# Kernel optimization log

Measured on AMD Instinct MI355X. Metric: run time of the kernel, lower is better.

The kernel has to match this reference:

```python
import jax, jax.numpy as jnp
import numpy as np

# ---- straight-through binary quantizers (custom VJP matches torch autograd.Functions) ----
@jax.custom_vjp
def bq(x):
    return jnp.sign(x)
def _bq_fwd(x):
    return jnp.sign(x), x
def _bq_bwd(x, g):
    return (g * ((x > -1.0) & (x < 1.0)).astype(g.dtype),)
bq.defvjp(_bq_fwd, _bq_bwd)

@jax.custom_vjp
def bq_quad(x):
    return jnp.sign(x)
def _bqq_fwd(x):
    return jnp.sign(x), x
def _bqq_bwd(x, g):
    return (jnp.maximum(2.0 - jnp.abs(2.0 * x), 0.0) * g,)
bq_quad.defvjp(_bqq_fwd, _bqq_bwd)

def bilinear(x, W, s, b):
    # BiLinear: row-centered sign weights scaled by learned per-row factor, sign activations
    Wc = W - jnp.mean(W, axis=-1, keepdims=True)
    Wb = s * bq(Wc)                      # (out, in)
    return bq(x) @ Wb.T + b

def selective_scan(u, delta, A, Bs, Cs, D, delta_bias):
    # u, delta: (B,K,Dn,L); A: (K,Dn,N); Bs,Cs: (B,K,N,L); D, delta_bias: (K,Dn)
    Bn, K, Dn, L = u.shape
    N = A.shape[-1]
    delta = jax.nn.softplus(delta + delta_bias[None, :, :, None])
    def step(h, inp):
        ut, dt, Bt, Ct = inp             # (B,K,Dn),(B,K,Dn),(B,K,N),(B,K,N)
        dA = jnp.exp(dt[..., None] * A[None])
        h = dA * h + (dt * ut)[..., None] * Bt[:, :, None, :]
        y = jnp.einsum('bkdn,bkn->bkd', h, Ct)
        return h, y
    h0 = jnp.zeros((Bn, K, Dn, N), u.dtype)
    _, ys = jax.lax.scan(step, h0,
                         (u.transpose(3, 0, 1, 2), delta.transpose(3, 0, 1, 2),
                          Bs.transpose(3, 0, 1, 2), Cs.transpose(3, 0, 1, 2)))
    y = ys.transpose(1, 2, 3, 0)         # (B,K,Dn,L)
    return y + D[None, :, :, None] * u

def _forward(x, W_in, b_in, s_in, move0_b, conv_W, conv_b, rp_b0, prelu_a, rp_b1,
             Wl, bl, sl, Wd, bd, sd, dt_bias, A_logs, Ds, ln_w, ln_b, W_out, b_out, s_out):
    Bn, H, Wi, dm = x.shape
    Dn = conv_W.shape[0]
    K = 4
    N = A_logs.shape[1]
    R = Wd.shape[2]
    L = H * Wi
    xz = bilinear(x, W_in, s_in, b_in)                  # (B,H,W,2*Dn)
    xp, z = jnp.split(xz, 2, axis=-1)
    xc = xp.transpose(0, 3, 1, 2)                       # (B,Dn,H,W)
    # BConv2d: move0 bias -> sign (quad STE) -> binary conv -> RPReLU -> residual
    t = bq_quad(xc + move0_b[None, :, None, None])
    sc = jax.lax.stop_gradient(jnp.mean(jnp.abs(conv_W), axis=(1, 2, 3), keepdims=True))
    cw = jnp.clip(conv_W, -1.0, 1.0)
    Wb = jax.lax.stop_gradient(sc * jnp.sign(conv_W) - cw) + cw
    t = jax.lax.conv_general_dilated(t, Wb, (1, 1), [(1, 1), (1, 1)],
                                     dimension_numbers=('NCHW', 'OIHW', 'NCHW'))
    t = t + conv_b[None, :, None, None]
    t = t + rp_b0[None, :, None, None]
    t = jnp.where(t >= 0, t, prelu_a[None, :, None, None] * t)
    t = t + rp_b1[None, :, None, None] + xc
    xconv = jax.nn.silu(t)
    # 4-direction scan inputs
    x_flat = xconv.reshape(Bn, Dn, L)
    x_tr = xconv.transpose(0, 1, 3, 2).reshape(Bn, Dn, L)
    x_hwwh = jnp.stack([x_flat, x_tr], axis=1)
    xs = jnp.concatenate([x_hwwh, jnp.flip(x_hwwh, axis=-1)], axis=1)   # (B,K,Dn,L)
    # NOTE: torch does .view(B,L,-1) on contiguous (B,Dn,L) slices = raw reshape (not transpose)
    xin = xs.reshape(Bn, K, L, Dn)
    x_dbl = jax.vmap(bilinear, in_axes=(1, 0, 0, 0), out_axes=1)(xin, Wl, sl, bl)  # (B,K,L,R+2N)
    x_dbl = x_dbl.transpose(0, 1, 3, 2)                                 # (B,K,R+2N,L)
    dts_r, Bs, Cs = jnp.split(x_dbl, [R, R + N], axis=2)
    dts_in = dts_r.reshape(Bn, K, L, R)  # raw reshape, matches torch .view
    dts = jax.vmap(bilinear, in_axes=(1, 0, 0, 0), out_axes=1)(dts_in, Wd, sd, bd)  # (B,K,L,Dn)
    dts = dts.transpose(0, 1, 3, 2)                                     # (B,K,Dn,L)
    A = -jnp.exp(A_logs).reshape(K, Dn, N)
    out_y = selective_scan(xs, dts, A, Bs, Cs, Ds.reshape(K, Dn), dt_bias.reshape(K, Dn))
    inv_y = jnp.flip(out_y[:, 2:4], axis=-1)
    wh_y = out_y[:, 1].reshape(Bn, Dn, Wi, H).transpose(0, 1, 3, 2).reshape(Bn, Dn, L)
    invwh_y = inv_y[:, 1].reshape(Bn, Dn, Wi, H).transpose(0, 1, 3, 2).reshape(Bn, Dn, L)
    y = out_y[:, 0] + inv_y[:, 0] + wh_y + invwh_y                      # (B,Dn,L)
    y = y.transpose(0, 2, 1).reshape(Bn, H, Wi, Dn)
    mu = jnp.mean(y, axis=-1, keepdims=True)
    var = jnp.var(y, axis=-1, keepdims=True)
    y = (y - mu) / jnp.sqrt(var + 1e-5) * ln_w + ln_b                   # LayerNorm eps=1e-5
    y = y * jax.nn.silu(z)
    return bilinear(y, W_out, s_out, b_out)

def setup_inputs():
    key = jax.random.key(0)
    ks = jax.random.split(key, 12)
    B, H, Wi, dm = 4, 64, 64, 96
    Dn, N, R, K = 192, 16, 6, 4
    u = lambda k, sh, a: jax.random.uniform(k, sh, jnp.float32, -a, a)
    x = jax.random.normal(ks[0], (B, H, Wi, dm), jnp.float32)
    W_in = u(ks[1], (2 * Dn, dm), 0.015)
    b_in = u(ks[2], (2 * Dn,), 0.01)
    s_in = jnp.mean(jnp.abs(W_in), axis=1, keepdims=True)
    move0_b = jnp.zeros((Dn,), jnp.float32)
    conv_W = 0.05 * jax.random.normal(ks[3], (Dn, Dn, 3, 3), jnp.float32)
    conv_b = u(ks[4], (Dn,), 0.01)
    rp_b0 = jnp.zeros((Dn,), jnp.float32)
    prelu_a = 0.25 * jnp.ones((Dn,), jnp.float32)
    rp_b1 = jnp.zeros((Dn,), jnp.float32)
    Wl = u(ks[5], (K, R + 2 * N, Dn), 0.015)
    bl = u(ks[6], (K, R + 2 * N), 0.01)
    sl = jnp.mean(jnp.abs(Wl), axis=2, keepdims=True)
    std = R ** -0.5
    Wd = u(ks[7], (K, Dn, R), std)
    bd = u(ks[8], (K, Dn), 0.01)
    sd = jnp.mean(jnp.abs(Wd), axis=2, keepdims=True)
    dt = jnp.exp(jax.random.uniform(ks[9], (K * Dn,), jnp.float32)
                 * (np.log(0.1) - np.log(0.001)) + np.log(0.001))
    dt = jnp.clip(dt, 1e-4, None)
    dt_bias = dt + jnp.log(-jnp.expm1(-dt))
    A_logs = jnp.tile(jnp.log(jnp.arange(1, N + 1, dtype=jnp.float32))[None, :], (K * Dn, 1))
    Ds = jnp.ones((K * Dn,), jnp.float32)
    ln_w = jnp.ones((Dn,), jnp.float32)
    ln_b = jnp.zeros((Dn,), jnp.float32)
    W_out = u(ks[10], (dm, Dn), 0.015)
    b_out = u(ks[11], (dm,), 0.01)
    s_out = jnp.mean(jnp.abs(W_out), axis=1, keepdims=True)
    return dict(x=x, W_in=W_in, b_in=b_in, s_in=s_in, move0_b=move0_b, conv_W=conv_W,
                conv_b=conv_b, rp_b0=rp_b0, prelu_a=prelu_a, rp_b1=rp_b1, Wl=Wl, bl=bl,
                sl=sl, Wd=Wd, bd=bd, sd=sd, dt_bias=dt_bias, A_logs=A_logs, Ds=Ds,
                ln_w=ln_w, ln_b=ln_b, W_out=W_out, b_out=b_out, s_out=s_out)

def reference(x, W_in, b_in, s_in, move0_b, conv_W, conv_b, rp_b0, prelu_a, rp_b1,
              Wl, bl, sl, Wd, bd, sd, dt_bias, A_logs, Ds, ln_w, ln_b, W_out, b_out, s_out):
    return _forward(x, W_in, b_in, s_in, move0_b, conv_W, conv_b, rp_b0, prelu_a, rp_b1,
                    Wl, bl, sl, Wd, bd, sd, dt_bias, A_logs, Ds, ln_w, ln_b, W_out, b_out, s_out)
```

## Files before the change

### kernel.cpp

```cpp
#include <hip/hip_runtime.h>
#include <math.h>
#include <stdint.h>

#define BB 4
#define HH 64
#define WW2 64
#define DM 96
#define DN 192
#define KK 4
#define NN 16
#define RR 6
#define LL 4096
#define RN 38

#define LOG2E 1.4426950408889634f
#define LN2   0.6931471805599453f

#define OFF_WDB      0
#define OFF_WCS      4608
#define OFF_WAUX     15360
#define OFF_WSC      16896
#define OFF_WBIB     17088
#define OFF_WOUTB    18240
#define OFF_WLBB     18816
#define OFF_XBP      19728
#define OFF_PXS      19728
#define OFF_PXIN     412944
#define OFF_XP       462096
#define OFF_XCONV    3607824
#define OFF_XCT      6753552
#define OFF_HEND     462096
#define OFF_YA       9899280
#define OFF_SSUM     22482192

#define PLANE 4356
#define NCH 128
#define CHUNK 32

__device__ __forceinline__ float softplusf(float v) {
  return fmaxf(v, 0.f) + LN2 * log2f(1.f + exp2f(-fabsf(v) * LOG2E));
}
__device__ __forceinline__ float siluf(float v) {
  return v / (1.f + expf(-v));
}
__device__ __forceinline__ float waveAllSum(float s) {
  #pragma unroll
  for (int off = 32; off; off >>= 1) s += __shfl_xor(s, off, 64);
  return s;
}

__global__ __launch_bounds__(64) void k_prep(
    const float* __restrict__ W_in, const float* __restrict__ s_in,
    const float* __restrict__ W_out, const float* __restrict__ s_out,
    const float* __restrict__ Wl, const float* __restrict__ sl,
    const float* __restrict__ Wd, const float* __restrict__ sd,
    const float* __restrict__ convW, float* __restrict__ ws) {
  __shared__ float srow[1728];
  int r = blockIdx.x, lane = threadIdx.x;
  if (r < 384) {
    const float* row = W_in + r * DM;
    float s = 0.f;
    for (int c = lane; c < DM; c += 64) s += row[c];
    s = waveAllSum(s);
    float mean = s / (float)DM;
    if (lane < 3) {
      uint32_t wv = 0;
      #pragma unroll
      for (int i = 0; i < 32; ++i) wv |= (row[lane * 32 + i] - mean > 0.f ? 1u : 0u) << i;
      ((uint32_t*)(ws + OFF_WBIB))[r * 3 + lane] = wv;
    }
  } else if (r < 480) {
    int m = r - 384;
    const float* row = W_out + m * DN;
    float s = 0.f;
    for (int c = lane; c < DN; c += 64) s += row[c];
    s = waveAllSum(s);
    float mean = s / (float)DN;
    if (lane < 6) {
      uint32_t wv = 0;
      #pragma unroll
      for (int i = 0; i < 32; ++i) wv |= (row[lane * 32 + i] - mean > 0.f ? 1u : 0u) << i;
      ((uint32_t*)(ws + OFF_WOUTB))[m * 6 + lane] = wv;
    }
  } else if (r < 632) {
    int idx = r - 480;
    const float* row = Wl + idx * DN;
    float s = 0.f;
    for (int c = lane; c < DN; c += 64) s += row[c];
    s = waveAllSum(s);
    float mean = s / (float)DN;
    if (lane < 6) {
      uint32_t wv = 0;
      #pragma unroll
      for (int i = 0; i < 32; ++i) wv |= (row[lane * 32 + i] - mean > 0.f ? 1u : 0u) << i;
      ((uint32_t*)(ws + OFF_WLBB))[idx * 6 + lane] = wv;
    }
  } else if (r < 1400) {
    int idx = r - 632;
    const float* row = Wd + idx * RR;
    float s = (lane < RR) ? row[lane] : 0.f;
    s = waveAllSum(s);
    float mean = s / (float)RR;
    unsigned long long mb = __ballot((lane < RR) && (row[lane] - mean > 0.f));
    if (lane == 0) {
      ((uint32_t*)(ws + OFF_WDB))[idx] = (uint32_t)mb & 0x3Fu;
      (ws + OFF_WDB)[768 + idx] = sd[idx];
    }
  } else if (r < 1592) {
    int o = r - 1400;
    const float* row = convW + o * 1728;
    float s = 0.f;
    for (int j = lane; j < 1728; j += 64) {
      float v = row[j];
      srow[j] = v;
      s += fabsf(v);
    }
    s = waveAllSum(s);
    __syncthreads();
    float sc = s / 1728.f;
    uint32_t* wb = (uint32_t*)(ws + OFF_WCS);
    int* aux = (int*)(ws + OFF_WAUX);
    float* scf = ws + OFF_WSC;
    uint32_t word = 0;
    if (lane < 54) {
      int cw = lane / 9, tap = lane % 9;
      #pragma unroll
      for (int i = 0; i < 32; ++i)
        word |= (srow[(cw * 32 + i) * 9 + tap] > 0.f ? 1u : 0u) << i;
      wb[o * 56 + lane] = word;
    } else if (lane < 56) {
      wb[o * 56 + lane] = 0u;
    }
    int pc = (lane < 54) ? 2 * (int)__popc(word) - 32 : 0;
    int tapid = lane % 9;
    int wst = 0;
    #pragma unroll
    for (int cw = 0; cw < 6; ++cw) wst += __shfl(pc, cw * 9 + tapid, 64);
    int w_t[9];
    #pragma unroll
    for (int t9 = 0; t9 < 9; ++t9) w_t[t9] = __shfl(wst, t9, 64);
    if (lane == 0) {
      aux[o * 8 + 0] = w_t[0] + w_t[3] + w_t[6];
      aux[o * 8 + 1] = w_t[2] + w_t[5] + w_t[8];
      aux[o * 8 + 2] = w_t[0] + w_t[1] + w_t[2];
      aux[o * 8 + 3] = w_t[6] + w_t[7] + w_t[8];
      aux[o * 8 + 4] = w_t[0];
      aux[o * 8 + 5] = w_t[2];
      aux[o * 8 + 6] = w_t[6];
      aux[o * 8 + 7] = w_t[8];
      scf[o] = sc;
    }
  } else {
    int p = r - 1592;
    uint32_t* plane = (uint32_t*)(ws + OFF_XBP) + (size_t)p * PLANE;
    for (int i = lane; i < 66; i += 64) {
      plane[i] = 0u;
      plane[65 * 66 + i] = 0u;
    }
    for (int i = lane; i < 64; i += 64) {
      plane[(i + 1) * 66] = 0u;
      plane[(i + 1) * 66 + 65] = 0u;
    }
  }
}

__global__ __launch_bounds__(384) void k_bilin_in(
    const float* __restrict__ x, const float* __restrict__ b_in,
    const float* __restrict__ s_in, const float* __restrict__ move0,
    const float* __restrict__ ws, float* __restrict__ xp,
    uint32_t* __restrict__ pxin, uint32_t* __restrict__ xb) {
  __shared__ uint32_t spx[16 * 3];
  __shared__ float sxz[192 * 17];
  __shared__ float smv[DN];
  int p0 = blockIdx.x * 16;
  if (threadIdx.x < 48) {
    int pix = threadIdx.x / 3, wd = threadIdx.x % 3;
    const float* base = x + (size_t)(p0 + pix) * DM + wd * 32;
    uint32_t wv = 0;
    #pragma unroll
    for (int i = 0; i < 32; ++i) wv |= (base[i] > 0.f ? 1u : 0u) << i;
    spx[pix * 3 + wd] = wv;
  }
  if (threadIdx.x < DN) smv[threadIdx.x] = move0[threadIdx.x];
  __syncthreads();
  int half = threadIdx.x / 192;
  int o = threadIdx.x - half * 192;
  uint32_t w0, w1, w2;
  {
    const uint32_t* wb = (const uint32_t*)(ws + OFF_WBIB) + o * 3;
    w0 = wb[0]; w1 = wb[1]; w2 = wb[2];
  }
  float bias = b_in[o], sc = s_in[o];
  #pragma unroll
  for (int pp = 0; pp < 8; ++pp) {
    int pix = half * 8 + pp;
    int P = (int)__popc(spx[pix * 3 + 0] ^ w0) + (int)__popc(spx[pix * 3 + 1] ^ w1) +
            (int)__popc(spx[pix * 3 + 2] ^ w2);
    sxz[o * 17 + pix] = bias + sc * (float)(DM - 2 * P);
  }
  __syncthreads();
  int b = p0 >> 12, l0 = p0 & 4095;
  for (int f = threadIdx.x; f < DN * 16; f += 384) {
    int od = f >> 4, pix = f & 15;
    xp[((size_t)(b * DN + od)) * LL + l0 + pix] = sxz[od * 17 + pix];
  }
  if (threadIdx.x < 48) {
    int pix = threadIdx.x / 3, wd = threadIdx.x % 3;
    pxin[(size_t)(p0 + pix) * 3 + wd] = spx[pix * 3 + wd];
  }
  if (threadIdx.x < 96) {
    int pix = threadIdx.x / 6, cw = threadIdx.x % 6;
    uint32_t wv = 0;
    #pragma unroll
    for (int i = 0; i < 32; ++i) {
      int dch = cw * 32 + i;
      wv |= ((sxz[dch * 17 + pix] + smv[dch] > 0.f) ? 1u : 0u) << i;
    }
    int l = l0 + pix, h = l >> 6, w = l & 63;
    uint32_t* plane = xb + (size_t)(b * 6 + cw) * PLANE;
    plane[(h + 1) * 66 + 1 + w] = wv;
  }
}

__global__ __launch_bounds__(256) void k_conv(
    const uint32_t* __restrict__ xb, const float* __restrict__ xc,
    const uint32_t* __restrict__ wbits, const int* __restrict__ aux,
    const float* __restrict__ scf, const float* __restrict__ conv_b,
    const float* __restrict__ rp_b0, const float* __restrict__ prelu_a,
    const float* __restrict__ rp_b1, float* __restrict__ xconv) {
  int ocg = blockIdx.x & 3;
  int og = (blockIdx.x >> 2) & 3;
  int stripe = (blockIdx.x >> 4) & 15;
  int b = blockIdx.x >> 8;
  int w = threadIdx.x & 63, r = threadIdx.x >> 6;
  int h = stripe * 4 + r;
  int obase = og * 48 + ocg * 12;

  __shared__ uint32_t swb[12 * 56];
  __shared__ int saux[12 * 8];
  __shared__ float sconst[12 * 4];
  for (int i = threadIdx.x; i < 12 * 56; i += 256) swb[i] = wbits[obase * 56 + i];
  for (int i = threadIdx.x; i < 12 * 8; i += 256) saux[i] = aux[obase * 8 + i];
  if (threadIdx.x < 12) {
    int o = obase + threadIdx.x;
    sconst[threadIdx.x * 4 + 0] = scf[o];
    sconst[threadIdx.x * 4 + 1] = conv_b[o] + rp_b0[o];
    sconst[threadIdx.x * 4 + 2] = prelu_a[o];
    sconst[threadIdx.x * 4 + 3] = rp_b1[o];
  }

  uint32_t xw[6][9];
  const uint32_t* xpb = xb + (size_t)b * 6 * PLANE;
  #pragma unroll
  for (int cw = 0; cw < 6; ++cw) {
    const uint32_t* plane = xpb + cw * PLANE + (h + 1) * 66 + (w + 1);
    #pragma unroll
    for (int dy = 0; dy < 3; ++dy) {
      #pragma unroll
      for (int dx = 0; dx < 3; ++dx)
        xw[cw][dy * 3 + dx] = plane[(dy - 1) * 66 + (dx - 1)];
    }
  }
  bool isL = (w == 0), isR = (w == 63);
  bool isT = (h == 0), isB = (h == 63);
  const float* xcp = xc + ((size_t)(b * DN + obase)) * LL + h * 64 + w;
  float* xop = xconv + ((size_t)(b * DN + obase)) * LL + h * 64 + w;
  __syncthreads();

  #pragma unroll 1
  for (int oc = 0; oc < 12; ++oc) {
    const uint32_t* wp = &swb[oc * 56];
    int P = 0;
    #pragma unroll
    for (int cw = 0; cw < 6; ++cw) {
      int pp = 0;
      #pragma unroll
      for (int t = 0; t < 9; ++t) pp += (int)__popc(wp[cw * 9 + t] ^ xw[cw][t]);
      P += pp;
    }
    int corr = isL ? saux[oc * 8 + 0] : (isR ? saux[oc * 8 + 1] : 0);
    if (isT) {
      corr += saux[oc * 8 + 2];
      if (isL) corr -= saux[oc * 8 + 4];
      if (isR) corr -= saux[oc * 8 + 5];
    }
    if (isB) {
      corr += saux[oc * 8 + 3];
      if (isL) corr -= saux[oc * 8 + 6];
      if (isR) corr -= saux[oc * 8 + 7];
    }
    float acc = sconst[oc * 4 + 0] * (float)(1728 - 2 * P + corr);
    float t = acc + sconst[oc * 4 + 1];
    t = (t >= 0.f) ? t : sconst[oc * 4 + 2] * t;
    t += sconst[oc * 4 + 3] + *xcp;
    *xop = siluf(t);
    xcp += LL; xop += LL;
  }
}

__global__ __launch_bounds__(256) void k_bits_xpose(const float* __restrict__ xconv,
                                                    uint32_t* __restrict__ pxs,
                                                    float* __restrict__ xct) {
  __shared__ float tile[64][65];
  if (blockIdx.x < 768) {
    int bd = blockIdx.x;
    int b = bd / DN, dch = bd - b * DN;
    const float* img = xconv + (size_t)bd * LL;
    for (int i = threadIdx.x; i < LL; i += 256)
      tile[i >> 6][i & 63] = img[i];
    __syncthreads();
    int lane = threadIdx.x & 63;
    #pragma unroll
    for (int k = 0; k < 4; ++k) {
      size_t wbase = ((size_t)((b * KK + k) * DN + dch)) * 128;
      for (int j = threadIdx.x; j < LL; j += 256) {
        float v;
        if (k == 0)      v = tile[j >> 6][j & 63];
        else if (k == 1) v = tile[j & 63][j >> 6];
        else if (k == 2) { int t2 = 4095 - j; v = tile[t2 >> 6][t2 & 63]; }
        else             { int t2 = 4095 - j; v = tile[t2 & 63][t2 >> 6]; }
        unsigned long long m = __ballot(v > 0.f);
        if (lane == 0)       pxs[wbase + (j >> 5)] = (uint32_t)m;
        else if (lane == 32) pxs[wbase + (j >> 5)] = (uint32_t)(m >> 32);
      }
    }
  } else {
    int idx = blockIdx.x - 768;
    int ts = idx & 63;
    int rest = idx >> 6;
    int dg = rest % 3;
    int b = rest / 3;
    int d0 = dg * 64, t0 = ts * 64;
    for (int i = threadIdx.x; i < 4096; i += 256) {
      int dd = i >> 6, tt = i & 63;
      tile[dd][tt] = xconv[((size_t)(b * DN + d0 + dd)) * LL + t0 + tt];
    }
    __syncthreads();
    for (int i = threadIdx.x; i < 4096; i += 256) {
      int tt = i >> 6, dd = i & 63;
      xct[((size_t)(b * LL + t0 + tt)) * DN + d0 + dd] = tile[dd][tt];
    }
  }
}

__device__ __forceinline__ void rpowers(float r, float* a) {
  float r2 = r * r, r3 = r2 * r, r4 = r2 * r2, r8 = r4 * r4;
  a[0] = r;       a[1] = r2;      a[2] = r3;      a[3] = r4;
  a[4] = r4 * r;  a[5] = r4 * r2; a[6] = r4 * r3; a[7] = r8;
  a[8] = r8 * r;  a[9] = r8 * r2; a[10] = r8 * r3; a[11] = r8 * r4;
  a[12] = r8 * a[4]; a[13] = r8 * a[5]; a[14] = r8 * a[6]; a[15] = r8 * r8;
}

__device__ __forceinline__ int rowstep(int k) {
  return (k == 0) ? DN : (k == 1) ? 64 * DN : (k == 2) ? -DN : -64 * DN;
}
__device__ __forceinline__ int rowbase(int k, int tb) {
  int r0 = (k >= 2) ? (4095 - tb) : tb;
  if (k & 1) r0 = ((r0 & 63) << 6) | (r0 >> 6);
  return r0 * DN;
}

__global__ __launch_bounds__(192) void k_scan_a(
    const float* __restrict__ xct, const uint32_t* __restrict__ pxs,
    const float* __restrict__ ws, const float* __restrict__ bl,
    const float* __restrict__ sl, const float* __restrict__ bd,
    const float* __restrict__ dt_bias, const float* __restrict__ A_logs,
    float* __restrict__ hend, float* __restrict__ Ssum) {
  int c = blockIdx.x & (NCH - 1);
  int bk = blockIdx.x >> 7;
  int k = bk & 3, b = bk >> 2;
  int d = threadIdx.x;
  int t0 = c << 5;
  __shared__ uint32_t sdtm[CHUNK];
  __shared__ uint32_t spxr[CHUNK * 6];
  __shared__ uint32_t swl[RN * 6];
  __shared__ float sblv[RN], sslv[RN];
  __shared__ float4 sB4[CHUNK * 4];
  __shared__ float sDV[7 * 192], sR[7 * 192];
  float* sBf = (float*)sB4;
  const uint32_t* ppx = pxs + (size_t)bk * 24576;
  spxr[d] = ppx[t0 * 6 + d];
  for (int i = d; i < RN * 6; i += 192) swl[i] = ((const uint32_t*)(ws + OFF_WLBB))[k * RN * 6 + i];
  if (d < RN) {
    sblv[d] = bl[k * RN + d];
    sslv[d] = sl[k * RN + d];
  }
  __syncthreads();
  if (d < CHUNK) {
    uint32_t m = 0;
    int fbase = (t0 + d) * 6;
    #pragma unroll
    for (int r = 0; r < 6; ++r) {
      int f = fbase + r;
      int o = f >> 12, l = f & 4095;
      const uint32_t* prow = ppx + l * 6;
      int P = 0;
      #pragma unroll
      for (int j = 0; j < 6; ++j) P += (int)__popc(prow[j] ^ swl[o * 6 + j]);
      float val = sblv[o] + sslv[o] * (float)(DN - 2 * P);
      m |= (val > 0.f ? 1u : 0u) << r;
    }
    sdtm[d] = m;
  }
  for (int i = d; i < CHUNK * 16; i += 192) {
    int t = i >> 4, n = i & 15;
    int o = RR + n;
    int P = 0;
    #pragma unroll
    for (int j = 0; j < 6; ++j) P += (int)__popc(spxr[t * 6 + j] ^ swl[o * 6 + j]);
    sBf[t * 16 + n] = sblv[o] + sslv[o] * (float)(DN - 2 * P);
  }
  uint32_t w6 = ((const uint32_t*)(ws + OFF_WDB))[k * DN + d];
  float sdvv = (ws + OFF_WDB)[768 + k * DN + d];
  float biasd = bd[k * DN + d] + dt_bias[k * DN + d];
  #pragma unroll
  for (int pc = 0; pc < 7; ++pc) {
    float dv = softplusf(biasd + sdvv * (float)(RR - 2 * pc));
    sDV[pc * 192 + d] = dv;
    sR[pc * 192 + d] = exp2f(-dv * LOG2E);
  }
  float Araw[16];
  bool fok = true;
  {
    const float* ap = A_logs + (k * DN + d) * NN;
    #pragma unroll
    for (int n = 0; n < NN; ++n) {
      Araw[n] = -expf(ap[n]);
      fok = fok && (fabsf(Araw[n] + (float)(n + 1)) < 1e-3f);
    }
  }
  bool fastpath = (__ballot(fok) == ~0ull);
  float An[16];
  if (!fastpath) {
    #pragma unroll
    for (int n = 0; n < NN; ++n) An[n] = Araw[n] * LOG2E;
  }
  float h[16];
  #pragma unroll
  for (int n = 0; n < NN; ++n) h[n] = 0.f;
  float S = 0.f;
  int ubase = b * (LL * DN) + d;
  int rstep = rowstep(k);
  __syncthreads();
  #pragma unroll 1
  for (int seg = 0; seg < 4; ++seg) {
    int rbase = rowbase(k, t0 + seg * 8);
    float uu[8];
    #pragma unroll
    for (int i = 0; i < 8; ++i) uu[i] = xct[ubase + rbase + i * rstep];
    #pragma unroll
    for (int i = 0; i < 8; ++i) {
      int t = seg * 8 + i;
      float uv = uu[i];
      int pc = (int)__popc(sdtm[t] ^ w6);
      float dv = sDV[pc * 192 + d];
      S += dv;
      float du = dv * uv;
      if (fastpath) {
        float rv = sR[pc * 192 + d];
        float a[16];
        rpowers(rv, a);
        #pragma unroll
        for (int g = 0; g < 4; ++g) {
          float4 bv = sB4[t * 4 + g];
          h[4 * g + 0] = a[4 * g + 0] * h[4 * g + 0] + du * bv.x;
          h[4 * g + 1] = a[4 * g + 1] * h[4 * g + 1] + du * bv.y;
          h[4 * g + 2] = a[4 * g + 2] * h[4 * g + 2] + du * bv.z;
          h[4 * g + 3] = a[4 * g + 3] * h[4 * g + 3] + du * bv.w;
        }
      } else {
        #pragma unroll
        for (int g = 0; g < 4; ++g) {
          float4 bv = sB4[t * 4 + g];
          float a0 = exp2f(dv * An[4 * g + 0]);
          float a1 = exp2f(dv * An[4 * g + 1]);
          float a2 = exp2f(dv * An[4 * g + 2]);
          float a3 = exp2f(dv * An[4 * g + 3]);
          h[4 * g + 0] = a0 * h[4 * g + 0] + du * bv.x;
          h[4 * g + 1] = a1 * h[4 * g + 1] + du * bv.y;
          h[4 * g + 2] = a2 * h[4 * g + 2] + du * bv.z;
          h[4 * g + 3] = a3 * h[4 * g + 3] + du * bv.w;
        }
      }
    }
  }
  float* hp = hend + (size_t)c * 49152 + (size_t)(bk * DN + d) * 16;
  #pragma unroll
  for (int n = 0; n < NN; n += 4)
    *(float4*)(hp + n) = make_float4(h[n], h[n + 1], h[n + 2], h[n + 3]);
  Ssum[c * 3072 + bk * DN + d] = S;
}

__global__ __launch_bounds__(256) void k_scan_b(
    const float* __restrict__ A_logs, const float* __restrict__ Ssum,
    float* __restrict__ hend) {
  int tid = blockIdx.x * 256 + threadIdx.x;
  int bkd = tid >> 4, n = tid & 15;
  int bk = bkd / DN, d = bkd - bk * DN;
  int k = bk & 3;
  float An2 = -expf(A_logs[(k * DN + d) * NN + n]) * LOG2E;
  float h = 0.f;
  float Sc = Ssum[bkd];
  float he = hend[tid];
  #pragma unroll 1
  for (int c = 0; c < NCH; ++c) {
    float Sn = 0.f, hn = 0.f;
    if (c < NCH - 1) {
      Sn = Ssum[(c + 1) * 3072 + bkd];
      hn = hend[(size_t)(c + 1) * 49152 + tid];
    }
    hend[(size_t)c * 49152 + tid] = h;
    h = exp2f(An2 * Sc) * h + he;
    Sc = Sn; he = hn;
  }
}

__global__ __launch_bounds__(192) void k_scan_c(
    const float* __restrict__ xct, const uint32_t* __restrict__ pxs,
    const float* __restrict__ ws, const float* __restrict__ bl,
    const float* __restrict__ sl, const float* __restrict__ bd,
    const float* __restrict__ dt_bias, const float* __restrict__ A_logs,
    const float* __restrict__ Ds, float* __restrict__ yA,
    const float* __restrict__ h0buf) {
  int c = blockIdx.x & (NCH - 1);
  int bk = blockIdx.x >> 7;
  int k = bk & 3, b = bk >> 2;
  int d = threadIdx.x;
  int t0 = c << 5;
  __shared__ uint32_t sdtm[CHUNK];
  __shared__ uint32_t spxr[CHUNK * 6];
  __shared__ uint32_t swl[RN * 6];
  __shared__ float sblv[RN], sslv[RN];
  __shared__ float4 sB4[CHUNK * 4];
  __shared__ float4 sC4[CHUNK * 4];
  __shared__ float sDV[7 * 192], sR[7 * 192];
  float* sBf = (float*)sB4;
  float* sCf = (float*)sC4;
  const uint32_t* ppx = pxs + (size_t)bk * 24576;
  spxr[d] = ppx[t0 * 6 + d];
  for (int i = d; i < RN * 6; i += 192) swl[i] = ((const uint32_t*)(ws + OFF_WLBB))[k * RN * 6 + i];
  if (d < RN) {
    sblv[d] = bl[k * RN + d];
    sslv[d] = sl[k * RN + d];
  }
  __syncthreads();
  if (d < CHUNK) {
    uint32_t m = 0;
    int fbase = (t0 + d) * 6;
    #pragma unroll
    for (int r = 0; r < 6; ++r) {
      int f = fbase + r;
      int o = f >> 12, l = f & 4095;
      const uint32_t* prow = ppx + l * 6;
      int P = 0;
      #pragma unroll
      for (int j = 0; j < 6; ++j) P += (int)__popc(prow[j] ^ swl[o * 6 + j]);
      float val = sblv[o] + sslv[o] * (float)(DN - 2 * P);
      m |= (val > 0.f ? 1u : 0u) << r;
    }
    sdtm[d] = m;
  }
  for (int i = d; i < CHUNK * 32; i += 192) {
    int t = i >> 5, nn = i & 31;
    int o = RR + nn;
    int P = 0;
    #pragma unroll
    for (int j = 0; j < 6; ++j) P += (int)__popc(spxr[t * 6 + j] ^ swl[o * 6 + j]);
    float val = sblv[o] + sslv[o] * (float)(DN - 2 * P);
    if (nn < 16) sBf[t * 16 + nn] = val;
    else         sCf[t * 16 + (nn - 16)] = val;
  }
  uint32_t w6 = ((const uint32_t*)(ws + OFF_WDB))[k * DN + d];
  float sdvv = (ws + OFF_WDB)[768 + k * DN + d];
  float biasd = bd[k * DN + d] + dt_bias[k * DN + d];
  float Dd = Ds[k * DN + d];
  #pragma unroll
  for (int pc = 0; pc < 7; ++pc) {
    float dv = softplusf(biasd + sdvv * (float)(RR - 2 * pc));
    sDV[pc * 192 + d] = dv;
    sR[pc * 192 + d] = exp2f(-dv * LOG2E);
  }
  float Araw[16];
  bool fok = true;
  {
    const float* ap = A_logs + (k * DN + d) * NN;
    #pragma unroll
    for (int n = 0; n < NN; ++n) {
      Araw[n] = -expf(ap[n]);
      fok = fok && (fabsf(Araw[n] + (float)(n + 1)) < 1e-3f);
    }
  }
  bool fastpath = (__ballot(fok) == ~0ull);
  float An[16];
  if (!fastpath) {
    #pragma unroll
    for (int n = 0; n < NN; ++n) An[n] = Araw[n] * LOG2E;
  }
  float h[16];
  {
    const float* hp = h0buf + (size_t)c * 49152 + (size_t)(bk * DN + d) * 16;
    #pragma unroll
    for (int n = 0; n < NN; n += 4) {
      float4 v = *(const float4*)(hp + n);
      h[n] = v.x; h[n + 1] = v.y; h[n + 2] = v.z; h[n + 3] = v.w;
    }
  }
  int ubase = b * (LL * DN) + d;
  int ybase = bk * (LL * DN) + d;
  int rstep = rowstep(k);
  __syncthreads();
  #pragma unroll 1
  for (int seg = 0; seg < 4; ++seg) {
    int rbase = rowbase(k, t0 + seg * 8);
    float uu[8];
    #pragma unroll
    for (int i = 0; i < 8; ++i) uu[i] = xct[ubase + rbase + i * rstep];
    #pragma unroll
    for (int i = 0; i < 8; ++i) {
      int t = seg * 8 + i;
      float uv = uu[i];
      int pc = (int)__popc(sdtm[t] ^ w6);
      float dv = sDV[pc * 192 + d];
      float du = dv * uv;
      float p[4];
      #pragma unroll
      for (int g = 0; g < 4; ++g) p[g] = 0.f;
      if (fastpath) {
        float rv = sR[pc * 192 + d];
        float a[16];
        rpowers(rv, a);
        #pragma unroll
        for (int g = 0; g < 4; ++g) {
          float4 bv = sB4[t * 4 + g];
          float4 cv = sC4[t * 4 + g];
          h[4 * g + 0] = a[4 * g + 0] * h[4 * g + 0] + du * bv.x;
          h[4 * g + 1] = a[4 * g + 1] * h[4 * g + 1] + du * bv.y;
          h[4 * g + 2] = a[4 * g + 2] * h[4 * g + 2] + du * bv.z;
          h[4 * g + 3] = a[4 * g + 3] * h[4 * g + 3] + du * bv.w;
          p[g] += cv.x * h[4 * g + 0];
          p[g] += cv.y * h[4 * g + 1];
          p[g] += cv.z * h[4 * g + 2];
          p[g] += cv.w * h[4 * g + 3];
        }
      } else {
        #pragma unroll
        for (int g = 0; g < 4; ++g) {
          float4 bv = sB4[t * 4 + g];
          float4 cv = sC4[t * 4 + g];
          float a0 = exp2f(dv * An[4 * g + 0]);
          float a1 = exp2f(dv * An[4 * g + 1]);
          float a2 = exp2f(dv * An[4 * g + 2]);
          float a3 = exp2f(dv * An[4 * g + 3]);
          h[4 * g + 0] = a0 * h[4 * g + 0] + du * bv.x;
          h[4 * g + 1] = a1 * h[4 * g + 1] + du * bv.y;
          h[4 * g + 2] = a2 * h[4 * g + 2] + du * bv.z;
          h[4 * g + 3] = a3 * h[4 * g + 3] + du * bv.w;
          p[g] += cv.x * h[4 * g + 0];
          p[g] += cv.y * h[4 * g + 1];
          p[g] += cv.z * h[4 * g + 2];
          p[g] += cv.w * h[4 * g + 3];
        }
      }
      float yv = Dd * uv + ((p[0] + p[1]) + (p[2] + p[3]));
      yA[ybase + rbase + i * rstep] = yv;
    }
  }
}

__global__ __launch_bounds__(256) void k_ln_out(
    const float* __restrict__ yA, const uint32_t* __restrict__ pxin,
    const float* __restrict__ b_in, const float* __restrict__ s_in,
    const float* __restrict__ ln_w, const float* __restrict__ ln_b,
    const float* __restrict__ ws, const float* __restrict__ b_out,
    const float* __restrict__ s_out, float* __restrict__ out) {
  __shared__ float ty[16 * 193];
  __shared__ float ps[256];
  __shared__ float smu[16], srs[16];
  __shared__ float slw[DN], slb[DN];
  __shared__ uint32_t ybits[16 * 6];
  __shared__ uint32_t swo[96 * 6];
  __shared__ float sb[96], ssc[96];
  __shared__ uint32_t szw[DN * 3];
  __shared__ float szb[DN], szs[DN];
  __shared__ uint32_t spxt[16 * 3];
  int b = blockIdx.x >> 8;
  int l0 = (blockIdx.x & 255) << 4;
  if (threadIdx.x < DN) {
    slw[threadIdx.x] = ln_w[threadIdx.x];
    slb[threadIdx.x] = ln_b[threadIdx.x];
    szb[threadIdx.x] = b_in[DN + threadIdx.x];
    szs[threadIdx.x] = s_in[DN + threadIdx.x];
  }
  for (int i = threadIdx.x; i < 96 * 6; i += 256) swo[i] = ((const uint32_t*)(ws + OFF_WOUTB))[i];
  for (int i = threadIdx.x; i < DN * 3; i += 256) szw[i] = ((const uint32_t*)(ws + OFF_WBIB))[DN * 3 + i];
  if (threadIdx.x < 96) {
    sb[threadIdx.x] = b_out[threadIdx.x];
    ssc[threadIdx.x] = s_out[threadIdx.x];
  }
  if (threadIdx.x < 48) spxt[threadIdx.x] = pxin[(size_t)(b * LL + l0) * 3 + threadIdx.x];
  const float* y0 = yA + (size_t)(b * 4 + 0) * (LL * DN) + (size_t)l0 * DN;
  const float* y1 = yA + (size_t)(b * 4 + 1) * (LL * DN) + (size_t)l0 * DN;
  const float* y2 = yA + (size_t)(b * 4 + 2) * (LL * DN) + (size_t)l0 * DN;
  const float* y3 = yA + (size_t)(b * 4 + 3) * (LL * DN) + (size_t)l0 * DN;
  for (int i = threadIdx.x; i < 16 * DN; i += 256) {
    int lc = i / DN, dd = i - lc * DN;
    size_t off = (size_t)lc * DN + dd;
    ty[lc * 193 + dd] = y0[off] + y1[off] + y2[off] + y3[off];
  }
  __syncthreads();
  int lc = threadIdx.x & 15, part = threadIdx.x >> 4;
  float s = 0.f;
  for (int d = part * 12; d < part * 12 + 12; ++d) s += ty[lc * 193 + d];
  ps[threadIdx.x] = s;
  __syncthreads();
  if (threadIdx.x < 16) {
    float m = 0.f;
    #pragma unroll
    for (int p = 0; p < 16; ++p) m += ps[p * 16 + threadIdx.x];
    smu[threadIdx.x] = m / (float)DN;
  }
  __syncthreads();
  float mu = smu[lc];
  float q = 0.f;
  for (int d = part * 12; d < part * 12 + 12; ++d) {
    float v = ty[lc * 193 + d] - mu; q += v * v;
  }
  ps[threadIdx.x] = q;
  __syncthreads();
  if (threadIdx.x < 16) {
    float vv = 0.f;
    #pragma unroll
    for (int p = 0; p < 16; ++p) vv += ps[p * 16 + threadIdx.x];
    srs[threadIdx.x] = rsqrtf(vv / (float)DN + 1e-5f);
  }
  __syncthreads();
  if (threadIdx.x < 16 * 6) {
    int lc2 = threadIdx.x / 6, wd = threadIdx.x % 6;
    float mu2 = smu[lc2], rs2 = srs[lc2];
    uint32_t px0 = spxt[lc2 * 3 + 0], px1 = spxt[lc2 * 3 + 1], px2 = spxt[lc2 * 3 + 2];
    uint32_t wv = 0;
    #pragma unroll
    for (int i = 0; i < 32; ++i) {
      int dd = wd * 32 + i;
      float lnv = (ty[lc2 * 193 + dd] - mu2) * rs2 * slw[dd] + slb[dd];
      int P = (int)__popc(px0 ^ szw[dd * 3 + 0]) + (int)__popc(px1 ^ szw[dd * 3 + 1]) +
              (int)__popc(px2 ^ szw[dd * 3 + 2]);
      float zv = szb[dd] + szs[dd] * (float)(DM - 2 * P);
      wv |= ((lnv * zv > 0.f) ? 1u : 0u) << i;
    }
    ybits[lc2 * 6 + wd] = wv;
  }
  __syncthreads();
  float* op = out + (size_t)(b * LL + l0) * DM;
  for (int oi = threadIdx.x; oi < 16 * DM; oi += 256) {
    int pr = oi / DM, m = oi % DM;
    int P = 0;
    #pragma unroll
    for (int j = 0; j < 6; ++j) P += (int)__popc(ybits[pr * 6 + j] ^ swo[m * 6 + j]);
    op[(size_t)pr * DM + m] = sb[m] + ssc[m] * (float)(DN - 2 * P);
  }
}

extern "C" void kernel_launch(void* const* d_in, const int* in_sizes, int n_in,
                              void* d_out, int out_size, void* d_ws, size_t ws_size,
                              hipStream_t stream) {
  const float* x       = (const float*)d_in[0];
  const float* W_in    = (const float*)d_in[1];
  const float* b_in    = (const float*)d_in[2];
  const float* s_in    = (const float*)d_in[3];
  const float* move0_b = (const float*)d_in[4];
  const float* conv_W  = (const float*)d_in[5];
  const float* conv_b  = (const float*)d_in[6];
  const float* rp_b0   = (const float*)d_in[7];
  const float* prelu_a = (const float*)d_in[8];
  const float* rp_b1   = (const float*)d_in[9];
  const float* Wl      = (const float*)d_in[10];
  const float* bl      = (const float*)d_in[11];
  const float* sl      = (const float*)d_in[12];
  const float* Wd      = (const float*)d_in[13];
  const float* bd      = (const float*)d_in[14];
  const float* sd      = (const float*)d_in[15];
  const float* dt_bias = (const float*)d_in[16];
  const float* A_logs  = (const float*)d_in[17];
  const float* Ds      = (const float*)d_in[18];
  const float* ln_w    = (const float*)d_in[19];
  const float* ln_b    = (const float*)d_in[20];
  const float* W_out   = (const float*)d_in[21];
  const float* b_out   = (const float*)d_in[22];
  const float* s_out   = (const float*)d_in[23];
  float* ws  = (float*)d_ws;
  float* out = (float*)d_out;

  hipLaunchKernelGGL(k_prep, dim3(1616), dim3(64), 0, stream,
                     W_in, s_in, W_out, s_out, Wl, sl, Wd, sd, conv_W, ws);
  hipLaunchKernelGGL(k_bilin_in, dim3(1024), dim3(384), 0, stream,
                     x, b_in, s_in, move0_b, ws, ws + OFF_XP,
                     (uint32_t*)(ws + OFF_PXIN), (uint32_t*)(ws + OFF_XBP));
  hipLaunchKernelGGL(k_conv, dim3(1024), dim3(256), 0, stream,
                     (const uint32_t*)(ws + OFF_XBP), ws + OFF_XP,
                     (const uint32_t*)(ws + OFF_WCS), (const int*)(ws + OFF_WAUX),
                     ws + OFF_WSC, conv_b, rp_b0, prelu_a, rp_b1,
                     ws + OFF_XCONV);
  hipLaunchKernelGGL(k_bits_xpose, dim3(1536), dim3(256), 0, stream,
                     ws + OFF_XCONV, (uint32_t*)(ws + OFF_PXS), ws + OFF_XCT);
  hipLaunchKernelGGL(k_scan_a, dim3(2048), dim3(192), 0, stream,
                     ws + OFF_XCT, (const uint32_t*)(ws + OFF_PXS), ws, bl, sl,
                     bd, dt_bias, A_logs, ws + OFF_HEND, ws + OFF_SSUM);
  hipLaunchKernelGGL(k_scan_b, dim3(192), dim3(256), 0, stream,
                     A_logs, ws + OFF_SSUM, ws + OFF_HEND);
  hipLaunchKernelGGL(k_scan_c, dim3(2048), dim3(192), 0, stream,
                     ws + OFF_XCT, (const uint32_t*)(ws + OFF_PXS), ws, bl, sl,
                     bd, dt_bias, A_logs, Ds, ws + OFF_YA, ws + OFF_HEND);
  hipLaunchKernelGGL(k_ln_out, dim3(1024), dim3(256), 0, stream,
                     ws + OFF_YA, (const uint32_t*)(ws + OFF_PXIN), b_in, s_in,
                     ln_w, ln_b, ws, b_out, s_out, out);
}
```

Measured before the change: 300.3 us.

## Split chunk-carry scan into two-level hierarchical scan across chunk groups

The sequential inter-chunk carry propagation (192 blocks walking 128 chunks serially) is replaced by a two-level scan. The first kernel scans 16-chunk groups independently and emits group-end states and summed decay exponents. The second kernel combines the preceding group states and adds the decayed carry into each chunk's start state. This exposes 8x more blocks and shortens the serial dependency chain, at the cost of an extra launch and an extra read-modify-write pass over hend.

New measurement: 277.3 us. 1.08x faster.

```diff
diff --git a/kernel.cpp b/kernel.cpp
--- a/kernel.cpp
+++ b/kernel.cpp
@@ -32,6 +32,8 @@
 #define OFF_HEND     462096
 #define OFF_YA       9899280
 #define OFF_SSUM     22482192
+#define OFF_GE       22875408
+#define OFF_GSG      23268624
 
 #define PLANE 4356
 #define NCH 128
@@ -491,27 +493,62 @@
   Ssum[c * 3072 + bk * DN + d] = S;
 }
 
-__global__ __launch_bounds__(256) void k_scan_b(
+__global__ __launch_bounds__(256) void k_scan_b1(
     const float* __restrict__ A_logs, const float* __restrict__ Ssum,
-    float* __restrict__ hend) {
-  int tid = blockIdx.x * 256 + threadIdx.x;
+    float* __restrict__ hend, float* __restrict__ gE, float* __restrict__ gSG) {
+  int g = blockIdx.x / 192;
+  int blk = blockIdx.x - g * 192;
+  int tid = blk * 256 + threadIdx.x;
   int bkd = tid >> 4, n = tid & 15;
   int bk = bkd / DN, d = bkd - bk * DN;
   int k = bk & 3;
   float An2 = -expf(A_logs[(k * DN + d) * NN + n]) * LOG2E;
-  float h = 0.f;
-  float Sc = Ssum[bkd];
-  float he = hend[tid];
+  int c0 = g * 16;
+  float E = 0.f, SG = 0.f;
+  float Sc = Ssum[c0 * 3072 + bkd];
+  float he = hend[(size_t)c0 * 49152 + tid];
   #pragma unroll 1
-  for (int c = 0; c < NCH; ++c) {
+  for (int j = 0; j < 16; ++j) {
+    int c = c0 + j;
     float Sn = 0.f, hn = 0.f;
-    if (c < NCH - 1) {
+    if (j < 15) {
       Sn = Ssum[(c + 1) * 3072 + bkd];
       hn = hend[(size_t)(c + 1) * 49152 + tid];
     }
-    hend[(size_t)c * 49152 + tid] = h;
-    h = exp2f(An2 * Sc) * h + he;
+    hend[(size_t)c * 49152 + tid] = E;
+    E = exp2f(An2 * Sc) * E + he;
+    SG += Sc;
     Sc = Sn; he = hn;
+  }
+  gE[(size_t)g * 49152 + tid] = E;
+  if (n == 0) gSG[g * 3072 + bkd] = SG;
+}
+
+__global__ __launch_bounds__(256) void k_scan_b2(
+    const float* __restrict__ A_logs, const float* __restrict__ Ssum,
+    float* __restrict__ hend, const float* __restrict__ gE,
+    const float* __restrict__ gSG) {
+  int g = blockIdx.x / 192;
+  if (g == 0) return;
+  int blk = blockIdx.x - g * 192;
+  int tid = blk * 256 + threadIdx.x;
+  int bkd = tid >> 4, n = tid & 15;
+  int bk = bkd / DN, d = bkd - bk * DN;
+  int k = bk & 3;
+  float An2 = -expf(A_logs[(k * DN + d) * NN + n]) * LOG2E;
+  float H = 0.f;
+  #pragma unroll 1
+  for (int j = 0; j < g; ++j) {
+    float Aj = exp2f(An2 * gSG[j * 3072 + bkd]);
+    H = Aj * H + gE[(size_t)j * 49152 + tid];
+  }
+  int c0 = g * 16;
+  float Spre = 0.f;
+  #pragma unroll 1
+  for (int j = 0; j < 16; ++j) {
+    int c = c0 + j;
+    hend[(size_t)c * 49152 + tid] += exp2f(An2 * Spre) * H;
+    Spre += Ssum[c * 3072 + bkd];
   }
 }
 
@@ -806,8 +843,10 @@
   hipLaunchKernelGGL(k_scan_a, dim3(2048), dim3(192), 0, stream,
                      ws + OFF_XCT, (const uint32_t*)(ws + OFF_PXS), ws, bl, sl,
                      bd, dt_bias, A_logs, ws + OFF_HEND, ws + OFF_SSUM);
-  hipLaunchKernelGGL(k_scan_b, dim3(192), dim3(256), 0, stream,
-                     A_logs, ws + OFF_SSUM, ws + OFF_HEND);
+  hipLaunchKernelGGL(k_scan_b1, dim3(1536), dim3(256), 0, stream,
+                     A_logs, ws + OFF_SSUM, ws + OFF_HEND, ws + OFF_GE, ws + OFF_GSG);
+  hipLaunchKernelGGL(k_scan_b2, dim3(1536), dim3(256), 0, stream,
+                     A_logs, ws + OFF_SSUM, ws + OFF_HEND, ws + OFF_GE, ws + OFF_GSG);
   hipLaunchKernelGGL(k_scan_c, dim3(2048), dim3(192), 0, stream,
                      ws + OFF_XCT, (const uint32_t*)(ws + OFF_PXS), ws, bl, sl,
                      bd, dt_bias, A_logs, Ds, ws + OFF_YA, ws + OFF_HEND);
```
